# Performance work log

Hardware: AMD Instinct MI355X
Metric: run time of the kernel (lower is better)

Reference implementation:

```python
import jax, jax.numpy as jnp
import numpy as np
import math

CHANNELS, BINS, HEADS, KSIZE = 4, 1024, 8, 3
ROT_DIM = BINS // HEADS // 2  # 64: rotate first half of each 128-dim head


def _rope(t):
    # t: [b, c, heads, w, d]; rotate first ROT_DIM dims, interleaved-pair style
    w = t.shape[-2]
    inv_freq = 1.0 / (10000.0 ** (jnp.arange(0, ROT_DIM, 2, dtype=jnp.float32) / ROT_DIM))
    freqs = jnp.arange(w, dtype=jnp.float32)[:, None] * inv_freq[None, :]   # [w, ROT_DIM//2]
    freqs = jnp.repeat(freqs, 2, axis=-1)                                    # [w, ROT_DIM]
    cos, sin = jnp.cos(freqs), jnp.sin(freqs)
    t_rot, t_pass = t[..., :ROT_DIM], t[..., ROT_DIM:]
    pair = t_rot.reshape(t_rot.shape[:-1] + (ROT_DIM // 2, 2))
    rotated = jnp.stack((-pair[..., 1], pair[..., 0]), axis=-1).reshape(t_rot.shape)
    return jnp.concatenate([t_rot * cos + rotated * sin, t_pass], axis=-1)


def _proj(x, w_lin, w_conv, b_conv):
    # MultichannelLinear: contract last dim with per-channel [out, in] weight
    y = jnp.einsum('bchi,coi->bcho', x, w_lin)
    # depthwise Conv2d, kernel (1, 3), padding (0, 1), groups = channels
    y = jax.lax.conv_general_dilated(
        y, w_conv, window_strides=(1, 1), padding=((0, 0), (1, 1)),
        dimension_numbers=('NCHW', 'OIHW', 'NCHW'), feature_group_count=CHANNELS)
    return y + b_conv[None, :, None, None]


def _split_heads(y):
    b, c, h, w = y.shape
    # transpose(2,3) -> [b,c,w,h]; reshape -> [b,c,w,heads,d]; permute -> [b,c,heads,w,d]
    return y.transpose(0, 1, 3, 2).reshape(b, c, w, HEADS, h // HEADS).transpose(0, 1, 3, 2, 4)


def setup_inputs() -> dict:
    key = jax.random.key(0)
    k1, k2, k3, k4, k5 = jax.random.split(key, 5)
    s_lin = 1.0 / math.sqrt(BINS)
    x = jax.random.normal(k1, (2, CHANNELS, BINS, BINS), dtype=jnp.float32)
    w_q_lin = jax.random.uniform(k2, (CHANNELS, BINS, BINS), jnp.float32, -s_lin, s_lin)
    w_q_conv = jax.random.uniform(k3, (CHANNELS, 1, 1, KSIZE), jnp.float32, -0.5, 0.5)
    b_q_conv = jax.random.uniform(k4, (CHANNELS,), jnp.float32, -0.5, 0.5)
    w_out = jax.random.uniform(k5, (CHANNELS, BINS, BINS), jnp.float32, -s_lin, s_lin)
    return {"x": x, "w_q_lin": w_q_lin, "w_q_conv": w_q_conv, "b_q_conv": b_q_conv, "w_out": w_out}


def reference(x, w_q_lin, w_q_conv, b_q_conv, w_out):
    b, c, h, w = x.shape
    # NOTE: original forward uses self.q_proj for q, k AND v (k_proj/v_proj unused)
    p = _proj(x, w_q_lin, w_q_conv, b_q_conv)          # [b,c,h,w]
    ph = _split_heads(p)                                # [b,c,heads,w,d]
    q = _rope(ph)
    k = _rope(ph)
    v = ph
    qk = jnp.einsum('bcnqd,bcnkd->bcnqk', q, k) / math.sqrt(h)
    a = jnp.einsum('bcnqk,bcnkd->bcnqd', jax.nn.softmax(qk, axis=-1), v)
    # merge heads back: [b,c,heads,w,d] -> [b,c,w,h] -> [b,c,h,w]
    a = a.transpose(0, 1, 3, 2, 4).reshape(b, c, w, h).transpose(0, 1, 3, 2)
    return jnp.einsum('bchi,coi->bcho', a, w_out)
```

## Files before the change

### kernel.cpp

```cpp
#include <hip/hip_runtime.h>
#include <cstdint>
#include <cstddef>

typedef __bf16 bf16;
typedef bf16 bf16x2 __attribute__((ext_vector_type(2)));
typedef bf16 bf16x4 __attribute__((ext_vector_type(4)));
typedef bf16 bf16x8 __attribute__((ext_vector_type(8)));
typedef float f32x4 __attribute__((ext_vector_type(4)));
typedef float f32x16 __attribute__((ext_vector_type(16)));

union B2F { float f; bf16x2 h; };

__device__ __forceinline__ void gload_lds16(const bf16* g, bf16* l) {
    __builtin_amdgcn_global_load_lds(
        (__attribute__((address_space(1))) void*)(uintptr_t)(g),
        (__attribute__((address_space(3))) void*)(l),
        16, 0, 0);
}

__global__ __launch_bounds__(256) void cvt_kernel(const float* __restrict__ in,
                                                  bf16* __restrict__ out, int n4) {
    int i = blockIdx.x * 256 + threadIdx.x;
    if (i >= n4) return;
    float4 v = ((const float4*)in)[i];
    bf16x4 o;
    o[0] = (bf16)v.x; o[1] = (bf16)v.y; o[2] = (bf16)v.z; o[3] = (bf16)v.w;
    *(bf16x4*)(out + (size_t)i * 4) = o;
}

__global__ __launch_bounds__(256) void rope_tab_kernel(float2* __restrict__ t) {
    int i = blockIdx.x * 256 + threadIdx.x;
    int w = i >> 5, j = i & 31;
    float inv = exp2f(-(float)j * (13.287712379549449f / 32.0f));
    float a = (float)w * inv;
    t[i] = make_float2(cosf(a), sinf(a));
}

template <bool F32OUT>
__global__ void __launch_bounds__(256) gemm_bt(const bf16* __restrict__ A,
                                               const bf16* __restrict__ B,
                                               void* __restrict__ Cout) {
    __shared__ alignas(16) bf16 As[128 * 64];
    __shared__ alignas(16) bf16 Bs[128 * 64];
    const int tid = threadIdx.x, lane = tid & 63, wave = tid >> 6;
    const int l15 = lane & 15, quad = lane >> 4;
    const int s = blockIdx.z;
    const bf16* Ab = A + ((size_t)s << 20) + (size_t)blockIdx.y * 128 * 1024;
    const bf16* Bb = B + ((size_t)(s & 3) << 20) + (size_t)blockIdx.x * 128 * 1024;
    const int wm = (wave >> 1) * 64, wn = (wave & 1) * 64;

    const f32x4 fzero = {0.f, 0.f, 0.f, 0.f};
    f32x4 acc[4][4];
    for (int i = 0; i < 4; ++i)
        for (int j = 0; j < 4; ++j) acc[i][j] = fzero;

    const int sr = wave * 8 + (lane >> 3);
    const int sc = (lane & 7) * 8;

    for (int kt = 0; kt < 16; ++kt) {
        __syncthreads();
        for (int it = 0; it < 4; ++it) {
            int r = it * 32 + sr;
            gload_lds16(Ab + (size_t)r * 1024 + kt * 64 + sc, As + r * 64 + sc);
            gload_lds16(Bb + (size_t)r * 1024 + kt * 64 + sc, Bs + r * 64 + sc);
        }
        __syncthreads();
        for (int kk = 0; kk < 2; ++kk) {
            bf16x8 af[4], bfr[4];
            for (int i = 0; i < 4; ++i)
                af[i] = *(const bf16x8*)(As + (wm + i * 16 + l15) * 64 + kk * 32 + quad * 8);
            for (int j = 0; j < 4; ++j)
                bfr[j] = *(const bf16x8*)(Bs + (wn + j * 16 + l15) * 64 + kk * 32 + quad * 8);
            for (int i = 0; i < 4; ++i)
                for (int j = 0; j < 4; ++j)
                    acc[i][j] = __builtin_amdgcn_mfma_f32_16x16x32_bf16(af[i], bfr[j],
                                                                        acc[i][j], 0, 0, 0);
        }
    }
    size_t cbase = ((size_t)s << 20) + (size_t)blockIdx.y * 128 * 1024 + blockIdx.x * 128;
    for (int i = 0; i < 4; ++i)
        for (int j = 0; j < 4; ++j) {
            int m = wm + i * 16 + quad * 4;
            int n = wn + j * 16 + l15;
            for (int r = 0; r < 4; ++r) {
                float v = acc[i][j][r];
                if (F32OUT)
                    ((float*)Cout)[cbase + (size_t)(m + r) * 1024 + n] = v;
                else
                    ((bf16*)Cout)[cbase + (size_t)(m + r) * 1024 + n] = (bf16)v;
            }
        }
}

__global__ void __launch_bounds__(256) conv_rope_kernel(
    const bf16* __restrict__ Yb, const float* __restrict__ wconv,
    const float* __restrict__ bconv, bf16* __restrict__ Qhat,
    bf16* __restrict__ Vhat, const float2* __restrict__ rtab) {
    __shared__ float Pt[32][260];
    const int s = blockIdx.z, cch = s & 3;
    const int h0 = blockIdx.y * 32, w0 = blockIdx.x * 256;
    const bf16* Y = Yb + ((size_t)s << 20);
    const float k0 = wconv[cch * 3], k1 = wconv[cch * 3 + 1], k2 = wconv[cch * 3 + 2];
    const float bias = bconv[cch];

    for (int it = 0; it < 4; ++it) {
        const int hh = threadIdx.x >> 3;
        const int wseg = (threadIdx.x & 7) + it * 8;
        const int h = h0 + hh, w = w0 + wseg * 8;
        const bf16* yrow = Y + ((size_t)h << 10);
        bf16x8 yv = *(const bf16x8*)(yrow + w);
        float yc[10];
        yc[0] = (w > 0) ? (float)yrow[w - 1] : 0.f;
        for (int i = 0; i < 8; ++i) yc[i + 1] = (float)yv[i];
        yc[9] = (w + 8 < 1024) ? (float)yrow[w + 8] : 0.f;
        bf16x8 pb;
        for (int i = 0; i < 8; ++i) {
            float p = fmaf(k0, yc[i], fmaf(k1, yc[i + 1], fmaf(k2, yc[i + 2], bias)));
            Pt[hh][wseg * 8 + i] = p;
            pb[i] = (bf16)p;
        }
        const int head = h >> 7, d = h & 127;
        *(bf16x8*)(Vhat + ((((size_t)s * 8 + head) * 128 + (w >> 3)) << 10) + d * 8) = pb;
    }
    __syncthreads();
    {
        const int dcb = threadIdx.x >> 6;
        const int head = h0 >> 7;
        const int d0 = (h0 & 127) + dcb * 8;
        const int hb0 = dcb * 8;
        for (int it = 0; it < 4; ++it) {
            const int wl = (threadIdx.x & 63) + it * 64;
            const int w = w0 + wl;
            float q[8];
            if (d0 < 64) {
                for (int j = 0; j < 8; j += 2) {
                    float2 cs = rtab[(w << 5) + ((d0 + j) >> 1)];
                    float a = Pt[hb0 + j][wl], b = Pt[hb0 + j + 1][wl];
                    q[j]     = fmaf(a, cs.x, -b * cs.y);
                    q[j + 1] = fmaf(b, cs.x,  a * cs.y);
                }
            } else {
                for (int j = 0; j < 8; ++j) q[j] = Pt[hb0 + j][wl];
            }
            bf16x8 qb;
            for (int j = 0; j < 8; ++j) qb[j] = (bf16)q[j];
            *(bf16x8*)(Qhat + ((((size_t)s * 8 + head) * 16 + (d0 >> 3)) << 13) +
                       (size_t)w * 8) = qb;
        }
    }
}

__global__ void __launch_bounds__(256, 2) attn_kernel(const bf16* __restrict__ Qhat,
                                                      const bf16* __restrict__ Vhat,
                                                      bf16* __restrict__ AO) {
    __shared__ alignas(16) char smem[66048];
    const int tid = threadIdx.x, lane = tid & 63, wave = tid >> 6;
    const int l31 = lane & 31, h = lane >> 5;
    const int b = blockIdx.x;
    const int sh = b & 63, qtile = b >> 6;
    const int s = sh >> 3, head = sh & 7, q0 = qtile * 128;
    const bf16* Qg = Qhat + (size_t)sh * 131072;
    const bf16* Vg = Vhat + (size_t)sh * 131072;

    const int myq = q0 + wave * 32 + l31;
    bf16x8 qf[8];
    for (int ks8 = 0; ks8 < 8; ++ks8)
        qf[ks8] = *(const bf16x8*)(Qg + (size_t)(ks8 * 2 + h) * 8192 + (size_t)myq * 8);

    f32x16 Oacc[4];
    for (int nt = 0; nt < 4; ++nt)
        for (int e = 0; e < 16; ++e) Oacc[nt][e] = 0.f;
    float lsum = 0.f;

    const float cexp = 1.4426950408889634f / 32.0f;

    auto stage = [&](int kt, int buf) {
        bf16* Ks = (bf16*)(smem + buf * 32768);
        bf16* Vs = Ks + 8192;
        for (int t = 0; t < 4; ++t) {
            int dc = wave * 4 + t;
            gload_lds16(Qg + (size_t)dc * 8192 + (size_t)(kt * 64 + lane) * 8,
                        Ks + (dc * 64 + lane) * 8);
            int wc = dc >> 1, half = dc & 1;
            gload_lds16(Vg + (size_t)(kt * 8 + wc) * 1024 + (size_t)(half * 64 + lane) * 8,
                        Vs + (wc * 128 + half * 64 + lane) * 8);
        }
    };

    stage(0, 0);
    for (int kt = 0; kt < 16; ++kt) {
        __syncthreads();
        if (kt < 15) stage(kt + 1, (kt + 1) & 1);
        bf16* Ks = (bf16*)(smem + (kt & 1) * 32768);
        bf16* Vs = Ks + 8192;

        f32x16 st[2];
        for (int e = 0; e < 16; ++e) { st[0][e] = 0.f; st[1][e] = 0.f; }
        for (int ks8 = 0; ks8 < 8; ++ks8) {
            bf16x8 kf0 = *(const bf16x8*)(Ks + ((ks8 * 2 + h) * 64 + l31) * 8);
            bf16x8 kf1 = *(const bf16x8*)(Ks + ((ks8 * 2 + h) * 64 + 32 + l31) * 8);
            st[0] = __builtin_amdgcn_mfma_f32_32x32x16_bf16(kf0, qf[ks8], st[0], 0, 0, 0);
            st[1] = __builtin_amdgcn_mfma_f32_32x32x16_bf16(kf1, qf[ks8], st[1], 0, 0, 0);
        }

        float pk[2][8], pkx[2][8];
        float lacc = 0.f;
        for (int mt = 0; mt < 2; ++mt)
            for (int k = 0; k < 8; ++k) {
                float a = exp2f(st[mt][2 * k] * cexp);
                float c = exp2f(st[mt][2 * k + 1] * cexp);
                lacc += a + c;
                B2F u; u.h = bf16x2{(bf16)a, (bf16)c};
                pk[mt][k] = u.f;
            }
        lsum += lacc;
        for (int mt = 0; mt < 2; ++mt)
            for (int k = 0; k < 8; ++k) pkx[mt][k] = __shfl_xor(pk[mt][k], 32);

        for (int ks = 0; ks < 4; ++ks) {
            const int bb = ks & 1, mt = ks >> 1;
            bf16x8 pf;
            float* pfF = (float*)&pf;
            pfF[0] = h ? pkx[mt][4 * bb + 2] : pk[mt][4 * bb + 0];
            pfF[1] = h ? pkx[mt][4 * bb + 3] : pk[mt][4 * bb + 1];
            pfF[2] = h ? pk[mt][4 * bb + 2] : pkx[mt][4 * bb + 0];
            pfF[3] = h ? pk[mt][4 * bb + 3] : pkx[mt][4 * bb + 1];
            for (int nt = 0; nt < 4; ++nt) {
                bf16x8 vf = *(const bf16x8*)(Vs + ((ks * 2 + h) * 128 + nt * 32 + l31) * 8);
                Oacc[nt] = __builtin_amdgcn_mfma_f32_32x32x16_bf16(pf, vf, Oacc[nt], 0, 0, 0);
            }
        }
    }

    lsum += __shfl_xor(lsum, 32);
    float* lsf = (float*)(smem + 65536) + wave * 32;
    if (lane < 32) lsf[lane] = 1.0f / lsum;
    f32x4 rv[4];
    __builtin_amdgcn_s_waitcnt(0);
    for (int rg = 0; rg < 4; ++rg)
        rv[rg] = *(const f32x4*)(lsf + 8 * rg + 4 * h);

    __syncthreads();
    bf16* Ot = (bf16*)smem;
    for (int nt = 0; nt < 4; ++nt) {
        int d = nt * 32 + l31;
        for (int rg = 0; rg < 4; ++rg) {
            int q = wave * 32 + 8 * rg + 4 * h;
            bf16x4 o4;
            for (int e = 0; e < 4; ++e)
                o4[e] = (bf16)(Oacc[nt][rg * 4 + e] * rv[rg][e]);
            *(bf16x4*)(Ot + d * 136 + q) = o4;
        }
    }
    __syncthreads();
    bf16* AOg = AO + ((size_t)s << 20);
    for (int it = 0; it < 8; ++it) {
        int d = it * 16 + (tid >> 4);
        int qc = (tid & 15) * 8;
        bf16x8 v = *(const bf16x8*)(Ot + d * 136 + qc);
        *(bf16x8*)(AOg + (size_t)(head * 128 + d) * 1024 + q0 + qc) = v;
    }
}

extern "C" void kernel_launch(void* const* d_in, const int* in_sizes, int n_in,
                              void* d_out, int out_size, void* d_ws, size_t ws_size,
                              hipStream_t stream) {
    const float* x  = (const float*)d_in[0];
    const float* wq = (const float*)d_in[1];
    const float* wc = (const float*)d_in[2];
    const float* bc = (const float*)d_in[3];
    const float* wo = (const float*)d_in[4];
    float* out = (float*)d_out;

    char* ws = (char*)d_ws;
    bf16* xb   = (bf16*)ws;
    bf16* wqb  = (bf16*)(ws + (16u << 20));
    bf16* wob  = (bf16*)(ws + (24u << 20));
    bf16* Yb   = (bf16*)(ws + (32u << 20));
    bf16* Qhat = (bf16*)(ws + (48u << 20));
    bf16* Vhat = (bf16*)(ws + (64u << 20));
    float2* rtab = (float2*)(ws + (80u << 20));
    bf16* AO   = xb;

    cvt_kernel<<<8192, 256, 0, stream>>>(x, xb, 2097152);
    cvt_kernel<<<4096, 256, 0, stream>>>(wq, wqb, 1048576);
    cvt_kernel<<<4096, 256, 0, stream>>>(wo, wob, 1048576);
    rope_tab_kernel<<<128, 256, 0, stream>>>(rtab);

    gemm_bt<false><<<dim3(8, 8, 8), 256, 0, stream>>>(xb, wqb, Yb);
    conv_rope_kernel<<<dim3(4, 32, 8), 256, 0, stream>>>(Yb, wc, bc, Qhat, Vhat, rtab);
    attn_kernel<<<512, 256, 0, stream>>>(Qhat, Vhat, AO);
    gemm_bt<true><<<dim3(8, 8, 8), 256, 0, stream>>>(AO, wob, out);
}
```

Measured before the change: 227.5 us.

## Read K/V directly from global in attention, fold softmax scale into Q, fuse conversions

The attention kernel stops staging K and V tiles in LDS through double-buffered async loads and instead reads MFMA operands straight from global memory. This cuts shared memory use and barriers, which may raise occupancy, but it relies on cache hits for the repeated K/V reads. The softmax scale and the log2e factor are folded into Q and K as a square-root scale during the conv/rope pass, which removes a multiply per score. The three fp32-to-bf16 conversion launches are merged into one kernel.

```diff
diff --git a/kernel.cpp b/kernel.cpp
--- a/kernel.cpp
+++ b/kernel.cpp
@@ -18,10 +18,18 @@
         16, 0, 0);
 }
 
-__global__ __launch_bounds__(256) void cvt_kernel(const float* __restrict__ in,
-                                                  bf16* __restrict__ out, int n4) {
+__global__ __launch_bounds__(256) void cvt3_kernel(const float* __restrict__ a,
+                                                   bf16* __restrict__ oa, int na4,
+                                                   const float* __restrict__ b,
+                                                   bf16* __restrict__ ob, int nb4,
+                                                   const float* __restrict__ c,
+                                                   bf16* __restrict__ oc, int nc4) {
     int i = blockIdx.x * 256 + threadIdx.x;
-    if (i >= n4) return;
+    const float* in; bf16* out;
+    if (i < na4) { in = a; out = oa; }
+    else if (i < na4 + nb4) { in = b; out = ob; i -= na4; }
+    else if (i < na4 + nb4 + nc4) { in = c; out = oc; i -= na4 + nb4; }
+    else return;
     float4 v = ((const float4*)in)[i];
     bf16x4 o;
     o[0] = (bf16)v.x; o[1] = (bf16)v.y; o[2] = (bf16)v.z; o[3] = (bf16)v.w;
@@ -102,6 +110,7 @@
     const bf16* Y = Yb + ((size_t)s << 20);
     const float k0 = wconv[cch * 3], k1 = wconv[cch * 3 + 1], k2 = wconv[cch * 3 + 2];
     const float bias = bconv[cch];
+    const float SQS = 0.21233045f;
 
     for (int it = 0; it < 4; ++it) {
         const int hh = threadIdx.x >> 3;
@@ -143,7 +152,7 @@
                 for (int j = 0; j < 8; ++j) q[j] = Pt[hb0 + j][wl];
             }
             bf16x8 qb;
-            for (int j = 0; j < 8; ++j) qb[j] = (bf16)q[j];
+            for (int j = 0; j < 8; ++j) qb[j] = (bf16)(q[j] * SQS);
             *(bf16x8*)(Qhat + ((((size_t)s * 8 + head) * 16 + (d0 >> 3)) << 13) +
                        (size_t)w * 8) = qb;
         }
@@ -153,7 +162,7 @@
 __global__ void __launch_bounds__(256, 2) attn_kernel(const bf16* __restrict__ Qhat,
                                                       const bf16* __restrict__ Vhat,
                                                       bf16* __restrict__ AO) {
-    __shared__ alignas(16) char smem[66048];
+    __shared__ alignas(16) char smem[35328];
     const int tid = threadIdx.x, lane = tid & 63, wave = tid >> 6;
     const int l31 = lane & 31, h = lane >> 5;
     const int b = blockIdx.x;
@@ -172,33 +181,13 @@
         for (int e = 0; e < 16; ++e) Oacc[nt][e] = 0.f;
     float lsum = 0.f;
 
-    const float cexp = 1.4426950408889634f / 32.0f;
-
-    auto stage = [&](int kt, int buf) {
-        bf16* Ks = (bf16*)(smem + buf * 32768);
-        bf16* Vs = Ks + 8192;
-        for (int t = 0; t < 4; ++t) {
-            int dc = wave * 4 + t;
-            gload_lds16(Qg + (size_t)dc * 8192 + (size_t)(kt * 64 + lane) * 8,
-                        Ks + (dc * 64 + lane) * 8);
-            int wc = dc >> 1, half = dc & 1;
-            gload_lds16(Vg + (size_t)(kt * 8 + wc) * 1024 + (size_t)(half * 64 + lane) * 8,
-                        Vs + (wc * 128 + half * 64 + lane) * 8);
-        }
-    };
-
-    stage(0, 0);
     for (int kt = 0; kt < 16; ++kt) {
-        __syncthreads();
-        if (kt < 15) stage(kt + 1, (kt + 1) & 1);
-        bf16* Ks = (bf16*)(smem + (kt & 1) * 32768);
-        bf16* Vs = Ks + 8192;
-
         f32x16 st[2];
         for (int e = 0; e < 16; ++e) { st[0][e] = 0.f; st[1][e] = 0.f; }
         for (int ks8 = 0; ks8 < 8; ++ks8) {
-            bf16x8 kf0 = *(const bf16x8*)(Ks + ((ks8 * 2 + h) * 64 + l31) * 8);
-            bf16x8 kf1 = *(const bf16x8*)(Ks + ((ks8 * 2 + h) * 64 + 32 + l31) * 8);
+            const bf16* kb = Qg + (size_t)(ks8 * 2 + h) * 8192 + (size_t)(kt * 64) * 8;
+            bf16x8 kf0 = *(const bf16x8*)(kb + (size_t)l31 * 8);
+            bf16x8 kf1 = *(const bf16x8*)(kb + (size_t)(32 + l31) * 8);
             st[0] = __builtin_amdgcn_mfma_f32_32x32x16_bf16(kf0, qf[ks8], st[0], 0, 0, 0);
             st[1] = __builtin_amdgcn_mfma_f32_32x32x16_bf16(kf1, qf[ks8], st[1], 0, 0, 0);
         }
@@ -207,8 +196,8 @@
         float lacc = 0.f;
         for (int mt = 0; mt < 2; ++mt)
             for (int k = 0; k < 8; ++k) {
-                float a = exp2f(st[mt][2 * k] * cexp);
-                float c = exp2f(st[mt][2 * k + 1] * cexp);
+                float a = exp2f(st[mt][2 * k]);
+                float c = exp2f(st[mt][2 * k + 1]);
                 lacc += a + c;
                 B2F u; u.h = bf16x2{(bf16)a, (bf16)c};
                 pk[mt][k] = u.f;
@@ -225,22 +214,22 @@
             pfF[1] = h ? pkx[mt][4 * bb + 3] : pk[mt][4 * bb + 1];
             pfF[2] = h ? pk[mt][4 * bb + 2] : pkx[mt][4 * bb + 0];
             pfF[3] = h ? pk[mt][4 * bb + 3] : pkx[mt][4 * bb + 1];
+            const bf16* vb = Vg + (size_t)(kt * 8 + ks * 2 + h) * 1024;
             for (int nt = 0; nt < 4; ++nt) {
-                bf16x8 vf = *(const bf16x8*)(Vs + ((ks * 2 + h) * 128 + nt * 32 + l31) * 8);
+                bf16x8 vf = *(const bf16x8*)(vb + (size_t)(nt * 32 + l31) * 8);
                 Oacc[nt] = __builtin_amdgcn_mfma_f32_32x32x16_bf16(pf, vf, Oacc[nt], 0, 0, 0);
             }
         }
     }
 
     lsum += __shfl_xor(lsum, 32);
-    float* lsf = (float*)(smem + 65536) + wave * 32;
+    float* lsf = (float*)(smem + 34816) + wave * 32;
     if (lane < 32) lsf[lane] = 1.0f / lsum;
     f32x4 rv[4];
     __builtin_amdgcn_s_waitcnt(0);
     for (int rg = 0; rg < 4; ++rg)
         rv[rg] = *(const f32x4*)(lsf + 8 * rg + 4 * h);
 
-    __syncthreads();
     bf16* Ot = (bf16*)smem;
     for (int nt = 0; nt < 4; ++nt) {
         int d = nt * 32 + l31;
@@ -282,9 +271,8 @@
     float2* rtab = (float2*)(ws + (80u << 20));
     bf16* AO   = xb;
 
-    cvt_kernel<<<8192, 256, 0, stream>>>(x, xb, 2097152);
-    cvt_kernel<<<4096, 256, 0, stream>>>(wq, wqb, 1048576);
-    cvt_kernel<<<4096, 256, 0, stream>>>(wo, wob, 1048576);
+    cvt3_kernel<<<16384, 256, 0, stream>>>(x, xb, 2097152, wq, wqb, 1048576,
+                                           wo, wob, 1048576);
     rope_tab_kernel<<<128, 256, 0, stream>>>(rtab);
 
     gemm_bt<false><<<dim3(8, 8, 8), 256, 0, stream>>>(xb, wqb, Yb);
```

New measurement: 283.7 us. +24.7%, slower.
